# Optimization experiments

Measured on AMD Instinct MI355X. Metric: run time of the kernel, lower is better.

## Reference

```python
import jax, jax.numpy as jnp
import numpy as np

H, D = 12, 768
DH = D // H  # 64
B, S = 2, 2048


def setup_inputs() -> dict:
    key = jax.random.key(0)
    ks = jax.random.split(key, 9)
    scale = 1.0 / np.sqrt(D)
    x = jax.random.normal(ks[0], (B, S, D), dtype=jnp.float32)
    # per-head QKV linears stacked over heads: W* [H, D, DH], b* [H, DH]
    Wq = jax.random.normal(ks[1], (H, D, DH), dtype=jnp.float32) * scale
    Wk = jax.random.normal(ks[2], (H, D, DH), dtype=jnp.float32) * scale
    Wv = jax.random.normal(ks[3], (H, D, DH), dtype=jnp.float32) * scale
    bq = jax.random.normal(ks[4], (H, DH), dtype=jnp.float32) * scale
    bk = jax.random.normal(ks[5], (H, DH), dtype=jnp.float32) * scale
    bv = jax.random.normal(ks[6], (H, DH), dtype=jnp.float32) * scale
    Wo = jax.random.normal(ks[7], (D, D), dtype=jnp.float32) * scale
    bo = jax.random.normal(ks[8], (D,), dtype=jnp.float32) * scale
    return {"x": x, "Wq": Wq, "Wk": Wk, "Wv": Wv, "bq": bq, "bk": bk,
            "bv": bv, "Wo": Wo, "bo": bo, "c": 0}


def reference(x, Wq, Wk, Wv, bq, bk, bv, Wo, bo, c):
    # x: [B,S,D] -> q/k/v: [B,H,S,DH]  (vectorized over the per-head loop)
    q = jnp.einsum('bsd,hde->bhse', x, Wq) + bq[None, :, None, :]
    k = jnp.einsum('bsd,hde->bhse', x, Wk) + bk[None, :, None, :]
    v = jnp.einsum('bsd,hde->bhse', x, Wv) + bv[None, :, None, :]
    scores = jnp.einsum('bhse,bhte->bhst', q, k) / jnp.sqrt(jnp.float32(DH))
    probs = jax.nn.softmax(scores, axis=-1)  # [B,H,S,S]
    # c==1 noise branch and dropout are identity in eval / c==0 setting
    ctx = jnp.einsum('bhst,bhte->bhse', probs, v)  # [B,H,S,DH]
    # concat heads along last dim (head order == torch cat order)
    ctx = jnp.transpose(ctx, (0, 2, 1, 3)).reshape(B, S, D)
    out = ctx @ Wo + bo
    return out
```

## Files before the change

kernel.cpp:

```cpp
#include <hip/hip_runtime.h>
#include <hip/hip_bf16.h>
#include <math.h>

#define NH   12
#define DM   768
#define DH   64
#define NB   2
#define SEQ  2048

typedef short s8v  __attribute__((ext_vector_type(8)));
typedef short s4v  __attribute__((ext_vector_type(4)));
typedef float f32x4 __attribute__((ext_vector_type(4)));
typedef float f32x16 __attribute__((ext_vector_type(16)));
typedef s8v bfrag;

#define MFMA(a,b,c)   __builtin_amdgcn_mfma_f32_16x16x32_bf16(a,b,c,0,0,0)
#define MFMA32(a,b,c) __builtin_amdgcn_mfma_f32_32x32x16_bf16(a,b,c,0,0,0)

#define QSCALE 0.18033688011112042f

__device__ __forceinline__ short f2bf(float f) {
    __hip_bfloat16 h = __float2bfloat16(f);
    return *(short*)&h;
}
__device__ __forceinline__ float bf2f(short s) {
    __hip_bfloat16 h; *(short*)&h = s;
    return __bfloat162float(h);
}
__device__ __forceinline__ float fexp2(float x) { return __builtin_amdgcn_exp2f(x); }
__device__ __forceinline__ unsigned pkbf(float a, float b) {
    unsigned r;
    asm("v_cvt_pk_bf16_f32 %0, %1, %2" : "=v"(r) : "v"(a), "v"(b));
    return r;
}
__device__ __forceinline__ void pl32swap(unsigned &a, unsigned &b) {
    asm volatile("v_permlane32_swap_b32 %0, %1" : "+v"(a), "+v"(b));
}
__device__ __forceinline__ bfrag mkfrag(unsigned d0, unsigned d1, unsigned d2, unsigned d3) {
    union { unsigned u[4]; bfrag f; } X;
    X.u[0] = d0; X.u[1] = d1; X.u[2] = d2; X.u[3] = d3;
    return X.f;
}

__global__ __launch_bounds__(256) void prep_all(
    const float* __restrict__ x,
    const float* __restrict__ Wq, const float* __restrict__ Wk,
    const float* __restrict__ Wv, const float* __restrict__ Wo,
    short* __restrict__ xbf, short* __restrict__ Wt,
    short* __restrict__ Wot)
{
    const int bid = blockIdx.x;
    const int t = threadIdx.x;
    __shared__ __align__(16) short T0[64 * 72];

    if (bid < 1536) {
        const size_t gid = (size_t)bid * 256 + t;
        const float4 a = ((const float4*)x)[gid * 2];
        const float4 b = ((const float4*)x)[gid * 2 + 1];
        s8v o;
        o[0]=f2bf(a.x); o[1]=f2bf(a.y); o[2]=f2bf(a.z); o[3]=f2bf(a.w);
        o[4]=f2bf(b.x); o[5]=f2bf(b.y); o[6]=f2bf(b.z); o[7]=f2bf(b.w);
        *(s8v*)&xbf[gid * 8] = o;
    } else if (bid < 1968) {
        const int id = bid - 1536;
        const int dt = id % 12, mh = id / 12;
        const int mat = mh / NH, h = mh % NH;
        const float* W = (mat == 0 ? Wq : mat == 1 ? Wk : Wv) + (size_t)h * DM * DH;
        {
            const int r = t >> 2, e0 = (t & 3) * 16;
            #pragma unroll
            for (int q = 0; q < 4; ++q) {
                const float4 a = *(const float4*)&W[(size_t)(dt * 64 + r) * DH + e0 + q * 4];
                s4v s; s[0]=f2bf(a.x); s[1]=f2bf(a.y); s[2]=f2bf(a.z); s[3]=f2bf(a.w);
                *(s4v*)&T0[r * 72 + e0 + q * 4] = s;
            }
        }
        __syncthreads();
        {
            const int e = t >> 2, r0 = (t & 3) * 16;
            s8v s0, s1;
            #pragma unroll
            for (int i = 0; i < 8; ++i) { s0[i] = T0[(r0 + i) * 72 + e]; s1[i] = T0[(r0 + 8 + i) * 72 + e]; }
            short* dst = Wt + (size_t)mh * DH * DM + (size_t)e * DM + dt * 64 + r0;
            *(s8v*)&dst[0] = s0; *(s8v*)&dst[8] = s1;
        }
    } else {
        const int id = bid - 1968;
        const int ntl = id % 12, ktl = id / 12;
        {
            const int r = t >> 2, n0q = (t & 3) * 16;
            #pragma unroll
            for (int q = 0; q < 4; ++q) {
                const float4 a = *(const float4*)&Wo[(size_t)(ktl * 64 + r) * DM + ntl * 64 + n0q + q * 4];
                s4v s; s[0]=f2bf(a.x); s[1]=f2bf(a.y); s[2]=f2bf(a.z); s[3]=f2bf(a.w);
                *(s4v*)&T0[r * 72 + n0q + q * 4] = s;
            }
        }
        __syncthreads();
        {
            const int n = t >> 2, r0 = (t & 3) * 16;
            s8v h0, h1;
            #pragma unroll
            for (int i = 0; i < 8; ++i) {
                h0[i] = T0[(r0 + i) * 72 + n];
                h1[i] = T0[(r0 + 8 + i) * 72 + n];
            }
            const size_t off = (size_t)(ntl * 64 + n) * DM + ktl * 64 + r0;
            *(s8v*)&Wot[off] = h0; *(s8v*)&Wot[off + 8] = h1;
        }
    }
}

__global__ __launch_bounds__(256) void qkv_mfma(
    const short* __restrict__ xbf, const short* __restrict__ Wt,
    const float* __restrict__ bq, const float* __restrict__ bk,
    const float* __restrict__ bv,
    short* __restrict__ qo, short* __restrict__ ko, short* __restrict__ vto)
{
    const int mt = blockIdx.x, sp = blockIdx.y;
    const int slab0 = sp * 2;
    const int mat = slab0 / NH, h0 = slab0 % NH;
    __shared__ __align__(16) short Al[128 * 72];
    __shared__ __align__(16) short Bl[128 * 72];
    const int t = threadIdx.x;
    const int w = t >> 6, lane = t & 63, l15 = lane & 15, g = lane >> 4;
    const int m0 = mt * 128;
    const short* Ws = Wt + (size_t)slab0 * DH * DM;

    f32x4 acc[2][8];
    #pragma unroll
    for (int i = 0; i < 2; ++i)
        #pragma unroll
        for (int j = 0; j < 8; ++j) acc[i][j] = 0.f;

    for (int kt = 0; kt < DM / 64; ++kt) {
        const int k0 = kt * 64;
        {
            const int row = t >> 1, kc = (t & 1) * 32;
            #pragma unroll
            for (int q = 0; q < 4; ++q)
                *(s8v*)&Al[row * 72 + kc + q * 8] = *(const s8v*)&xbf[(size_t)(m0 + row) * DM + k0 + kc + q * 8];
            #pragma unroll
            for (int q = 0; q < 4; ++q)
                *(s8v*)&Bl[row * 72 + kc + q * 8] = *(const s8v*)&Ws[(size_t)row * DM + k0 + kc + q * 8];
        }
        __syncthreads();
        #pragma unroll
        for (int kk = 0; kk < 2; ++kk) {
            bfrag a[2], b[8];
            #pragma unroll
            for (int i = 0; i < 2; ++i) a[i] = *(const bfrag*)&Al[(w * 32 + 16 * i + l15) * 72 + kk * 32 + 8 * g];
            #pragma unroll
            for (int j = 0; j < 8; ++j) b[j] = *(const bfrag*)&Bl[(16 * j + l15) * 72 + kk * 32 + 8 * g];
            #pragma unroll
            for (int i = 0; i < 2; ++i)
                #pragma unroll
                for (int j = 0; j < 8; ++j) acc[i][j] = MFMA(a[i], b[j], acc[i][j]);
        }
        __syncthreads();
    }

    const float* bias0 = (mat == 0 ? bq : mat == 1 ? bk : bv);
    const float scl = (mat == 0) ? QSCALE : 1.0f;
    #pragma unroll
    for (int j = 0; j < 8; ++j) {
        const int h = h0 + (j >> 2);
        const int n = (j & 3) * 16 + l15;
        const float bia = bias0[h * DH + n];
        if (mat < 2) {
            short* out = (mat == 0 ? qo : ko);
            #pragma unroll
            for (int i = 0; i < 2; ++i)
                #pragma unroll
                for (int r = 0; r < 4; ++r) {
                    const int m = m0 + w * 32 + 16 * i + 4 * g + r;
                    const int bb = m >> 11, s = m & (SEQ - 1);
                    out[(((size_t)bb * NH + h) * SEQ + s) * DH + n] = f2bf((acc[i][j][r] + bia) * scl);
                }
        } else {
            #pragma unroll
            for (int i = 0; i < 2; ++i) {
                const int m = m0 + w * 32 + 16 * i + 4 * g;
                const int bb = m >> 11, s = m & (SEQ - 1);
                s4v sv;
                #pragma unroll
                for (int r = 0; r < 4; ++r) sv[r] = f2bf(acc[i][j][r] + bia);
                *(s4v*)&vto[(((size_t)bb * NH + h) * DH + n) * SEQ + s] = sv;
            }
        }
    }
}

__global__ __launch_bounds__(256, 4) void attn_mfma(
    const short* __restrict__ qg, const short* __restrict__ kg,
    const short* __restrict__ vtg, short* __restrict__ ctx)
{
    const int n_  = blockIdx.x;
    const int xcd = n_ & 7, s_ = n_ >> 3;
    const int bh = xcd * 3 + (s_ % 3);
    const int qb = s_ / 3;
    const int b = bh / NH, h = bh % NH;

    __shared__ __align__(16) float Cb[4][3][16][64];
    __shared__ float Ls[4][2][64];

    const int t = threadIdx.x;
    const int w = t >> 6, l = t & 63, lo = l & 31, hi = l >> 5;
    const size_t base  = (size_t)bh * SEQ * DH;
    const size_t vbase = (size_t)bh * DH * SEQ;
    const int qbase = qb * 64;

    bfrag qf[2][4];
    #pragma unroll
    for (int qt = 0; qt < 2; ++qt)
        #pragma unroll
        for (int esl = 0; esl < 4; ++esl)
            qf[qt][esl] = *(const bfrag*)&qg[base + (size_t)(qbase + qt * 32 + lo) * DH + esl * 16 + hi * 8];

    f32x16 o00, o01, o10, o11;
    o00 = 0.f; o01 = 0.f; o10 = 0.f; o11 = 0.f;
    float ls0 = 0.f, ls1 = 0.f;

    const short* kbase_p = kg + base;
    const short* vbase_p = vtg + vbase;
    const int r0 = w * 512;

    auto SMPV = [&](const f32x16& s0, const f32x16& s1,
                    const bfrag& vf00, const bfrag& vf01,
                    const bfrag& vf10, const bfrag& vf11) {
        float p0[16], p1[16];
        #pragma unroll
        for (int i = 0; i < 16; ++i) p0[i] = fexp2(s0[i]);
        #pragma unroll
        for (int i = 0; i < 16; ++i) p1[i] = fexp2(s1[i]);
        ls0 += ((p0[0]+p0[1])+(p0[2]+p0[3])) + ((p0[4]+p0[5])+(p0[6]+p0[7]))
             + ((p0[8]+p0[9])+(p0[10]+p0[11])) + ((p0[12]+p0[13])+(p0[14]+p0[15]));
        ls1 += ((p1[0]+p1[1])+(p1[2]+p1[3])) + ((p1[4]+p1[5])+(p1[6]+p1[7]))
             + ((p1[8]+p1[9])+(p1[10]+p1[11])) + ((p1[12]+p1[13])+(p1[14]+p1[15]));

        unsigned a0 = pkbf(p0[0],  p0[1]),  a1 = pkbf(p0[2],  p0[3]);
        unsigned a2 = pkbf(p0[4],  p0[5]),  a3 = pkbf(p0[6],  p0[7]);
        unsigned c0_ = pkbf(p0[8], p0[9]),  c1_ = pkbf(p0[10], p0[11]);
        unsigned c2_ = pkbf(p0[12], p0[13]), c3_ = pkbf(p0[14], p0[15]);
        pl32swap(a0, a2); pl32swap(a1, a3); pl32swap(c0_, c2_); pl32swap(c1_, c3_);
        const bfrag pa00 = mkfrag(a0, a1, a2, a3);
        const bfrag pa01 = mkfrag(c0_, c1_, c2_, c3_);

        unsigned d0 = pkbf(p1[0],  p1[1]),  d1 = pkbf(p1[2],  p1[3]);
        unsigned d2 = pkbf(p1[4],  p1[5]),  d3 = pkbf(p1[6],  p1[7]);
        unsigned e0_ = pkbf(p1[8], p1[9]),  e1_ = pkbf(p1[10], p1[11]);
        unsigned e2_ = pkbf(p1[12], p1[13]), e3_ = pkbf(p1[14], p1[15]);
        pl32swap(d0, d2); pl32swap(d1, d3); pl32swap(e0_, e2_); pl32swap(e1_, e3_);
        const bfrag pa10 = mkfrag(d0, d1, d2, d3);
        const bfrag pa11 = mkfrag(e0_, e1_, e2_, e3_);

        __builtin_amdgcn_s_setprio(1);
        o00 = MFMA32(vf00, pa00, o00); o00 = MFMA32(vf01, pa01, o00);
        o10 = MFMA32(vf00, pa10, o10); o10 = MFMA32(vf01, pa11, o10);
        o01 = MFMA32(vf10, pa00, o01); o01 = MFMA32(vf11, pa01, o01);
        o11 = MFMA32(vf10, pa10, o11); o11 = MFMA32(vf11, pa11, o11);
        __builtin_amdgcn_s_setprio(0);
    };

    bfrag kfA[4], kfB[4];
    bfrag vfA[4], vfB[4];
    #pragma unroll
    for (int esl = 0; esl < 4; ++esl)
        kfA[esl] = *(const bfrag*)&kbase_p[(size_t)(r0 + lo) * DH + esl * 16 + hi * 8];
    vfA[0] = *(const bfrag*)&vbase_p[(size_t)lo * SEQ + r0 + hi * 8];
    vfA[1] = *(const bfrag*)&vbase_p[(size_t)lo * SEQ + r0 + 16 + hi * 8];
    vfA[2] = *(const bfrag*)&vbase_p[(size_t)(32 + lo) * SEQ + r0 + hi * 8];
    vfA[3] = *(const bfrag*)&vbase_p[(size_t)(32 + lo) * SEQ + r0 + 16 + hi * 8];

    for (int it2 = 0; it2 < 8; ++it2) {
        {
            const int it = 2 * it2;
            f32x16 s0, s1; s0 = 0.f; s1 = 0.f;
            __builtin_amdgcn_s_setprio(1);
            #pragma unroll
            for (int esl = 0; esl < 4; ++esl) {
                s0 = MFMA32(kfA[esl], qf[0][esl], s0);
                s1 = MFMA32(kfA[esl], qf[1][esl], s1);
            }
            __builtin_amdgcn_s_setprio(0);
            {
                const short* kp = kbase_p + (size_t)(r0 + (it + 1) * 32 + lo) * DH;
                #pragma unroll
                for (int esl = 0; esl < 4; ++esl)
                    kfB[esl] = *(const bfrag*)&kp[esl * 16 + hi * 8];
                const int vc = r0 + (it + 1) * 32;
                vfB[0] = *(const bfrag*)&vbase_p[(size_t)lo * SEQ + vc + hi * 8];
                vfB[1] = *(const bfrag*)&vbase_p[(size_t)lo * SEQ + vc + 16 + hi * 8];
                vfB[2] = *(const bfrag*)&vbase_p[(size_t)(32 + lo) * SEQ + vc + hi * 8];
                vfB[3] = *(const bfrag*)&vbase_p[(size_t)(32 + lo) * SEQ + vc + 16 + hi * 8];
            }
            SMPV(s0, s1, vfA[0], vfA[1], vfA[2], vfA[3]);
        }
        {
            const int it = 2 * it2 + 1;
            f32x16 s0, s1; s0 = 0.f; s1 = 0.f;
            __builtin_amdgcn_s_setprio(1);
            #pragma unroll
            for (int esl = 0; esl < 4; ++esl) {
                s0 = MFMA32(kfB[esl], qf[0][esl], s0);
                s1 = MFMA32(kfB[esl], qf[1][esl], s1);
            }
            __builtin_amdgcn_s_setprio(0);
            if (it2 < 7) {
                const short* kp = kbase_p + (size_t)(r0 + (it + 1) * 32 + lo) * DH;
                #pragma unroll
                for (int esl = 0; esl < 4; ++esl)
                    kfA[esl] = *(const bfrag*)&kp[esl * 16 + hi * 8];
                const int vc = r0 + (it + 1) * 32;
                vfA[0] = *(const bfrag*)&vbase_p[(size_t)lo * SEQ + vc + hi * 8];
                vfA[1] = *(const bfrag*)&vbase_p[(size_t)lo * SEQ + vc + 16 + hi * 8];
                vfA[2] = *(const bfrag*)&vbase_p[(size_t)(32 + lo) * SEQ + vc + hi * 8];
                vfA[3] = *(const bfrag*)&vbase_p[(size_t)(32 + lo) * SEQ + vc + 16 + hi * 8];
            }
            SMPV(s0, s1, vfB[0], vfB[1], vfB[2], vfB[3]);
        }
    }

    Ls[w][0][l] = ls0;
    Ls[w][1][l] = ls1;
    #pragma unroll
    for (int c = 0; c < 4; ++c) {
        if (c == w) continue;
        const int idx = (w < c) ? w : w - 1;
        const f32x16 src = (c == 0) ? o00 : (c == 1) ? o01 : (c == 2) ? o10 : o11;
        #pragma unroll
        for (int r = 0; r < 16; ++r)
            Cb[c][idx][r][l] = src[r];
    }
    __syncthreads();

    f32x16 oc = (w == 0) ? o00 : (w == 1) ? o01 : (w == 2) ? o10 : o11;
    #pragma unroll
    for (int idx = 0; idx < 3; ++idx)
        #pragma unroll
        for (int r = 0; r < 16; ++r)
            oc[r] += Cb[w][idx][r][l];
    const int mqt = w >> 1, met = w & 1;
    float lt = 0.f;
    #pragma unroll
    for (int w2 = 0; w2 < 4; ++w2)
        lt += Ls[w2][mqt][lo] + Ls[w2][mqt][lo + 32];
    const float inv = 1.0f / lt;
    __syncthreads();

    unsigned* l2 = (unsigned*)&Cb[0][0][0][0];
    #pragma unroll
    for (int rq = 0; rq < 4; ++rq) {
        #pragma unroll
        for (int ph = 0; ph < 2; ++ph) {
            const int r = 4 * rq + 2 * ph;
            const int col = met * 16 + 2 * hi + 4 * rq + ph;
            l2[(mqt * 32 + lo) * 33 + col] = pkbf(oc[r] * inv, oc[r + 1] * inv);
        }
    }
    __syncthreads();

    {
        const int row = t >> 2, ch = (t & 3) * 8;
        short* crow = &ctx[((size_t)b * SEQ + qbase + row) * DM + h * DH];
        #pragma unroll
        for (int q = 0; q < 2; ++q) {
            uint4 u;
            u.x = l2[row * 33 + ch + q * 4 + 0];
            u.y = l2[row * 33 + ch + q * 4 + 1];
            u.z = l2[row * 33 + ch + q * 4 + 2];
            u.w = l2[row * 33 + ch + q * 4 + 3];
            *(uint4*)&crow[(ch + q * 4) * 2] = u;
        }
    }
}

__global__ __launch_bounds__(256) void out_mfma(
    const short* __restrict__ ctx,
    const short* __restrict__ Wot,
    const float* __restrict__ bo, float* __restrict__ out)
{
    const int mt = blockIdx.x, ntl = blockIdx.y;
    __shared__ __align__(16) short Al[128 * 72];
    __shared__ __align__(16) short Bh[64 * 72];
    const int t = threadIdx.x;
    const int w = t >> 6, lane = t & 63, l15 = lane & 15, g = lane >> 4;
    const int m0 = mt * 128, n0 = ntl * 64;

    f32x4 acc[2][4];
    #pragma unroll
    for (int i = 0; i < 2; ++i)
        #pragma unroll
        for (int j = 0; j < 4; ++j) acc[i][j] = 0.f;

    for (int kt = 0; kt < DM / 64; ++kt) {
        const int k0 = kt * 64;
        {
            const int row = t >> 1, kc = (t & 1) * 32;
            #pragma unroll
            for (int q = 0; q < 4; ++q)
                *(s8v*)&Al[row * 72 + kc + q * 8] = *(const s8v*)&ctx[(size_t)(m0 + row) * DM + k0 + kc + q * 8];
        }
        {
            const int n = t >> 2, kc = (t & 3) * 16;
            *(s8v*)&Bh[n * 72 + kc]     = *(const s8v*)&Wot[(size_t)(n0 + n) * DM + k0 + kc];
            *(s8v*)&Bh[n * 72 + kc + 8] = *(const s8v*)&Wot[(size_t)(n0 + n) * DM + k0 + kc + 8];
        }
        __syncthreads();
        #pragma unroll
        for (int kk = 0; kk < 2; ++kk) {
            bfrag ah[2];
            #pragma unroll
            for (int i = 0; i < 2; ++i)
                ah[i] = *(const bfrag*)&Al[(w * 32 + 16 * i + l15) * 72 + kk * 32 + 8 * g];
            #pragma unroll
            for (int j = 0; j < 4; ++j) {
                const bfrag bh_ = *(const bfrag*)&Bh[(16 * j + l15) * 72 + kk * 32 + 8 * g];
                #pragma unroll
                for (int i = 0; i < 2; ++i)
                    acc[i][j] = MFMA(ah[i], bh_, acc[i][j]);
            }
        }
        __syncthreads();
    }

    #pragma unroll
    for (int j = 0; j < 4; ++j) {
        const int n = n0 + 16 * j + l15;
        const float bia = bo[n];
        #pragma unroll
        for (int i = 0; i < 2; ++i)
            #pragma unroll
            for (int r = 0; r < 4; ++r) {
                const int m = m0 + w * 32 + 16 * i + 4 * g + r;
                out[(size_t)m * DM + n] = acc[i][j][r] + bia;
            }
    }
}

extern "C" void kernel_launch(void* const* d_in, const int* in_sizes, int n_in,
                              void* d_out, int out_size, void* d_ws, size_t ws_size,
                              hipStream_t stream) {
    const float* x  = (const float*)d_in[0];
    const float* Wq = (const float*)d_in[1];
    const float* Wk = (const float*)d_in[2];
    const float* Wv = (const float*)d_in[3];
    const float* bq = (const float*)d_in[4];
    const float* bk = (const float*)d_in[5];
    const float* bv = (const float*)d_in[6];
    const float* Wo = (const float*)d_in[7];
    const float* bo = (const float*)d_in[8];
    float* out = (float*)d_out;

    char* ws = (char*)d_ws;
    short* xbf   = (short*)(ws);
    short* Wt    = (short*)(ws + 6291456);
    short* Wot   = (short*)(ws + 9830400);
    short* qb    = (short*)(ws + 12189696);
    short* kb    = (short*)(ws + 18481152);
    short* vtb   = (short*)(ws + 31064064);
    short* ctx   = (short*)(ws + 37355520);

    prep_all<<<2112, 256, 0, stream>>>(x, Wq, Wk, Wv, Wo, xbf, Wt, Wot);
    qkv_mfma<<<dim3(32, 18), 256, 0, stream>>>(xbf, Wt, bq, bk, bv, qb, kb, vtb);
    attn_mfma<<<768, 256, 0, stream>>>(qb, kb, vtb, ctx);
    out_mfma<<<dim3(32, 12), 256, 0, stream>>>(ctx, Wot, bo, out);
}
```

Baseline: 110.9 us.

## Store K and V in MFMA-fragment-tiled layout for contiguous attention loads

The QKV projection epilogue now writes K and transposed V in a blocked layout where each 32-key chunk holds pre-arranged MFMA fragments. The attention kernel can then load every K/V fragment as one contiguous 1 KB wavefront read (lane*8 shorts) instead of strided row or column gathers. This targets global memory coalescing and cache-line use in the attention inner loop. In exchange, the projection epilogue does more scattered stores for K.

```diff
diff --git a/kernel.cpp b/kernel.cpp
--- a/kernel.cpp
+++ b/kernel.cpp
@@ -161,31 +161,54 @@
     }
 
     const float* bias0 = (mat == 0 ? bq : mat == 1 ? bk : bv);
-    const float scl = (mat == 0) ? QSCALE : 1.0f;
-    #pragma unroll
-    for (int j = 0; j < 8; ++j) {
-        const int h = h0 + (j >> 2);
-        const int n = (j & 3) * 16 + l15;
-        const float bia = bias0[h * DH + n];
-        if (mat < 2) {
-            short* out = (mat == 0 ? qo : ko);
+    if (mat == 0) {
+        #pragma unroll
+        for (int j = 0; j < 8; ++j) {
+            const int h = h0 + (j >> 2);
+            const int n = (j & 3) * 16 + l15;
+            const float bia = bias0[h * DH + n];
             #pragma unroll
             for (int i = 0; i < 2; ++i)
                 #pragma unroll
                 for (int r = 0; r < 4; ++r) {
                     const int m = m0 + w * 32 + 16 * i + 4 * g + r;
                     const int bb = m >> 11, s = m & (SEQ - 1);
-                    out[(((size_t)bb * NH + h) * SEQ + s) * DH + n] = f2bf((acc[i][j][r] + bia) * scl);
+                    qo[(((size_t)bb * NH + h) * SEQ + s) * DH + n] = f2bf((acc[i][j][r] + bia) * QSCALE);
                 }
-        } else {
+        }
+    } else if (mat == 1) {
+        #pragma unroll
+        for (int j = 0; j < 8; ++j) {
+            const int h = h0 + (j >> 2);
+            const int n = (j & 3) * 16 + l15;
+            const float bia = bias0[h * DH + n];
+            #pragma unroll
+            for (int i = 0; i < 2; ++i)
+                #pragma unroll
+                for (int r = 0; r < 4; ++r) {
+                    const int m = m0 + w * 32 + 16 * i + 4 * g + r;
+                    const int bb = m >> 11, s = m & (SEQ - 1);
+                    ko[((size_t)bb * NH + h) * (SEQ * DH) + (size_t)(s >> 5) * 2048
+                       + (j & 3) * 512 + (l15 >> 3) * 256 + (s & 31) * 8 + (l15 & 7)]
+                        = f2bf(acc[i][j][r] + bia);
+                }
+        }
+    } else {
+        #pragma unroll
+        for (int j = 0; j < 8; ++j) {
+            const int h = h0 + (j >> 2);
+            const int n = (j & 3) * 16 + l15;
+            const float bia = bias0[h * DH + n];
             #pragma unroll
             for (int i = 0; i < 2; ++i) {
                 const int m = m0 + w * 32 + 16 * i + 4 * g;
-                const int bb = m >> 11, s = m & (SEQ - 1);
+                const int bb = m >> 11, k = m & (SEQ - 1);
                 s4v sv;
                 #pragma unroll
                 for (int r = 0; r < 4; ++r) sv[r] = f2bf(acc[i][j][r] + bia);
-                *(s4v*)&vto[(((size_t)bb * NH + h) * DH + n) * SEQ + s] = sv;
+                *(s4v*)&vto[((size_t)bb * NH + h) * (SEQ * DH) + (size_t)(k >> 5) * 2048
+                            + ((j & 3) >> 1) * 1024 + i * 512
+                            + (g >> 1) * 256 + ((j & 1) * 16 + l15) * 8 + (g & 1) * 4] = sv;
             }
         }
     }
@@ -207,7 +230,6 @@
     const int t = threadIdx.x;
     const int w = t >> 6, l = t & 63, lo = l & 31, hi = l >> 5;
     const size_t base  = (size_t)bh * SEQ * DH;
-    const size_t vbase = (size_t)bh * DH * SEQ;
     const int qbase = qb * 64;
 
     bfrag qf[2][4];
@@ -221,9 +243,9 @@
     o00 = 0.f; o01 = 0.f; o10 = 0.f; o11 = 0.f;
     float ls0 = 0.f, ls1 = 0.f;
 
-    const short* kbase_p = kg + base;
-    const short* vbase_p = vtg + vbase;
-    const int r0 = w * 512;
+    const short* kbp = kg + base;
+    const short* vbp = vtg + base;
+    const int kb0 = w * 16;
 
     auto SMPV = [&](const f32x16& s0, const f32x16& s1,
                     const bfrag& vf00, const bfrag& vf01,
@@ -266,11 +288,10 @@
     bfrag vfA[4], vfB[4];
     #pragma unroll
     for (int esl = 0; esl < 4; ++esl)
-        kfA[esl] = *(const bfrag*)&kbase_p[(size_t)(r0 + lo) * DH + esl * 16 + hi * 8];
-    vfA[0] = *(const bfrag*)&vbase_p[(size_t)lo * SEQ + r0 + hi * 8];
-    vfA[1] = *(const bfrag*)&vbase_p[(size_t)lo * SEQ + r0 + 16 + hi * 8];
-    vfA[2] = *(const bfrag*)&vbase_p[(size_t)(32 + lo) * SEQ + r0 + hi * 8];
-    vfA[3] = *(const bfrag*)&vbase_p[(size_t)(32 + lo) * SEQ + r0 + 16 + hi * 8];
+        kfA[esl] = *(const bfrag*)&kbp[(size_t)kb0 * 2048 + esl * 512 + l * 8];
+    #pragma unroll
+    for (int q = 0; q < 4; ++q)
+        vfA[q] = *(const bfrag*)&vbp[(size_t)kb0 * 2048 + q * 512 + l * 8];
 
     for (int it2 = 0; it2 < 8; ++it2) {
         {
@@ -284,15 +305,13 @@
             }
             __builtin_amdgcn_s_setprio(0);
             {
-                const short* kp = kbase_p + (size_t)(r0 + (it + 1) * 32 + lo) * DH;
+                const size_t co = (size_t)(kb0 + it + 1) * 2048;
                 #pragma unroll
                 for (int esl = 0; esl < 4; ++esl)
-                    kfB[esl] = *(const bfrag*)&kp[esl * 16 + hi * 8];
-                const int vc = r0 + (it + 1) * 32;
-                vfB[0] = *(const bfrag*)&vbase_p[(size_t)lo * SEQ + vc + hi * 8];
-                vfB[1] = *(const bfrag*)&vbase_p[(size_t)lo * SEQ + vc + 16 + hi * 8];
-                vfB[2] = *(const bfrag*)&vbase_p[(size_t)(32 + lo) * SEQ + vc + hi * 8];
-                vfB[3] = *(const bfrag*)&vbase_p[(size_t)(32 + lo) * SEQ + vc + 16 + hi * 8];
+                    kfB[esl] = *(const bfrag*)&kbp[co + esl * 512 + l * 8];
+                #pragma unroll
+                for (int q = 0; q < 4; ++q)
+                    vfB[q] = *(const bfrag*)&vbp[co + q * 512 + l * 8];
             }
             SMPV(s0, s1, vfA[0], vfA[1], vfA[2], vfA[3]);
         }
@@ -307,15 +326,13 @@
             }
             __builtin_amdgcn_s_setprio(0);
             if (it2 < 7) {
-                const short* kp = kbase_p + (size_t)(r0 + (it + 1) * 32 + lo) * DH;
+                const size_t co = (size_t)(kb0 + it + 1) * 2048;
                 #pragma unroll
                 for (int esl = 0; esl < 4; ++esl)
-                    kfA[esl] = *(const bfrag*)&kp[esl * 16 + hi * 8];
-                const int vc = r0 + (it + 1) * 32;
-                vfA[0] = *(const bfrag*)&vbase_p[(size_t)lo * SEQ + vc + hi * 8];
-                vfA[1] = *(const bfrag*)&vbase_p[(size_t)lo * SEQ + vc + 16 + hi * 8];
-                vfA[2] = *(const bfrag*)&vbase_p[(size_t)(32 + lo) * SEQ + vc + hi * 8];
-                vfA[3] = *(const bfrag*)&vbase_p[(size_t)(32 + lo) * SEQ + vc + 16 + hi * 8];
+                    kfA[esl] = *(const bfrag*)&kbp[co + esl * 512 + l * 8];
+                #pragma unroll
+                for (int q = 0; q < 4; ++q)
+                    vfA[q] = *(const bfrag*)&vbp[co + q * 512 + l * 8];
             }
             SMPV(s0, s1, vfB[0], vfB[1], vfB[2], vfB[3]);
         }
```

New measurement: 102.4 us (median of 3 runs). 1.08x faster.
